# Kernel tuning notes

Hardware: AMD Instinct MI355X
Metric: run time of the kernel (lower is better)

Reference implementation:

```python
import jax, jax.numpy as jnp
import numpy as np

N_ORDERS = 4  # edge groups processed sequentially by EmulsionConv


def setup_inputs() -> dict:
    key = jax.random.key(0)
    ks = jax.random.split(key, 12)
    N, E, D_IN, H, D_OUT, ED = 50000, 800000, 10, 64, 10, 1
    s = 0.1
    return {
        "x": jax.random.normal(ks[0], (N, D_IN), jnp.float32),
        "edge_index": jax.random.randint(ks[1], (2, E), 0, N, jnp.int32),
        "edge_features": jax.random.normal(ks[2], (E, ED), jnp.float32),
        "lin0_w": jax.random.normal(ks[3], (D_IN, H), jnp.float32) * s,
        "lin0_b": jnp.zeros((H,), jnp.float32),
        "lin1_w": jax.random.normal(ks[4], (H, H), jnp.float32) * s,
        "lin1_b": jnp.zeros((H,), jnp.float32),
        "lin2_w": jax.random.normal(ks[5], (H, H), jnp.float32) * s,
        "lin2_b": jnp.zeros((H,), jnp.float32),
        "em_w": jax.random.normal(ks[6], (3, 2 * H + ED, H), jnp.float32) * s,
        "em_b": jnp.zeros((3, H), jnp.float32),
        "ec_w": jax.random.normal(ks[7], (3, 2 * H, H), jnp.float32) * s,
        "ec_b": jnp.zeros((3, H), jnp.float32),
        "out_w": jax.random.normal(ks[8], (H, D_OUT), jnp.float32) * s,
        "out_b": jnp.zeros((D_OUT,), jnp.float32),
    }


def _emulsion_conv(x, edge_index, edge_features, w, b):
    # Sequential per-order gather -> MLP message -> scatter-add; direction=0 (aggregate at source).
    N = x.shape[0]
    E = edge_index.shape[1]
    per = E // N_ORDERS
    for i in range(N_ORDERS):
        sl = slice(i * per, (i + 1) * per)
        src = edge_index[0, sl]
        dst = edge_index[1, sl]
        x_j = x[src]  # [per, H]
        x_i = x[dst]  # [per, H]
        msg = jnp.concatenate([x_i, x_j - x_i, edge_features[sl]], axis=1)
        msg = jax.nn.relu(msg @ w + b)
        agg = jax.ops.segment_sum(msg, src, num_segments=N)
        x = (x + agg) / 2.0
    return x


def _edge_conv(x, edge_index, w, b):
    # EdgeConv: nn([x_i, x_j - x_i]) with max aggregation at target nodes.
    N = x.shape[0]
    src, dst = edge_index[0], edge_index[1]
    x_i = x[dst]
    x_j = x[src]
    msg = jax.nn.relu(jnp.concatenate([x_i, x_j - x_i], axis=1) @ w + b)
    agg = jax.ops.segment_max(msg, dst, num_segments=N)
    return jnp.where(jnp.isfinite(agg), agg, 0.0)  # empty segments -> 0


def reference(x, edge_index, edge_features,
              lin0_w, lin0_b, lin1_w, lin1_b, lin2_w, lin2_b,
              em_w, em_b, ec_w, ec_b, out_w, out_b):
    lin_ws = [lin0_w, lin1_w, lin2_w]
    lin_bs = [lin0_b, lin1_b, lin2_b]
    for i in range(3):
        x = jax.nn.relu(x @ lin_ws[i] + lin_bs[i])
        x = _emulsion_conv(x, edge_index, edge_features, em_w[i], em_b[i])
    for i in range(3):
        x = _edge_conv(x, edge_index, ec_w[i], ec_b[i])
    return x @ out_w + out_b
```

## Files before the change

kernel.cpp:

```cpp
#include <hip/hip_runtime.h>
#include <hip/hip_fp16.h>


#define NN 50000
#define NE 800000
#define PER 200000
#define HD 64
#define NKEY 250112

typedef _Float16 half8 __attribute__((ext_vector_type(8)));
typedef float float4v __attribute__((ext_vector_type(4)));

__global__ __launch_bounds__(256) void count_kernel(
        const int* __restrict__ ei, int* __restrict__ cnt,
        uchar2* __restrict__ rank) {
    int e = blockIdx.x * 256 + threadIdx.x;
    if (e >= NE) return;
    int src = ei[e];
    int dst = ei[NE + e];
    int o = e / PER;
    int r1 = atomicAdd(&cnt[o * NN + src], 1);
    int r2 = atomicAdd(&cnt[4 * NN + dst], 1);
    rank[e] = make_uchar2((unsigned char)r1, (unsigned char)r2);
}

__global__ __launch_bounds__(256) void scan_blk(
        const int* __restrict__ cnt, int* __restrict__ bsum) {
    __shared__ int s[256];
    int t = threadIdx.x;
    int i = blockIdx.x * 256 + t;
    int c = (i < NKEY) ? cnt[i] : 0;
    s[t] = c; __syncthreads();
    for (int d = 1; d < 256; d <<= 1) {
        int v = (t >= d) ? s[t - d] : 0;
        __syncthreads(); s[t] += v; __syncthreads();
    }
    if (t == 255) bsum[blockIdx.x] = s[255];
}

__global__ __launch_bounds__(1024) void scan_top(
        const int* __restrict__ bsum, int* __restrict__ bofs, int nb) {
    __shared__ int s[1024];
    int t = threadIdx.x;
    int c = (t < nb) ? bsum[t] : 0;
    s[t] = c; __syncthreads();
    for (int d = 1; d < 1024; d <<= 1) {
        int v = (t >= d) ? s[t - d] : 0;
        __syncthreads(); s[t] += v; __syncthreads();
    }
    if (t < nb) bofs[t] = s[t] - c;
}

__global__ __launch_bounds__(256) void scan_fin(
        const int* __restrict__ cnt, const int* __restrict__ bofs,
        int* __restrict__ ofs) {
    __shared__ int s[256];
    int t = threadIdx.x;
    int i = blockIdx.x * 256 + t;
    int c = (i < NKEY) ? cnt[i] : 0;
    s[t] = c; __syncthreads();
    for (int d = 1; d < 256; d <<= 1) {
        int v = (t >= d) ? s[t - d] : 0;
        __syncthreads(); s[t] += v; __syncthreads();
    }
    if (i < NKEY) ofs[i] = bofs[blockIdx.x] + s[t] - c;
}

__global__ __launch_bounds__(256) void fill_kernel(
        const int* __restrict__ ei, const float* __restrict__ ef,
        const int* __restrict__ ofs, const uchar2* __restrict__ rank,
        unsigned* __restrict__ em_val, int* __restrict__ ec_val) {
    int e = blockIdx.x * 256 + threadIdx.x;
    if (e >= NE) return;
    int src = ei[e];
    int dst = ei[NE + e];
    int o = e / PER;
    uchar2 r = rank[e];
    int p1 = ofs[o * NN + src] + r.x;
    unsigned short eb = __half_as_ushort(__float2half_rn(ef[e]));
    em_val[p1] = ((unsigned)dst << 16) | (unsigned)eb;
    int p2 = ofs[4 * NN + dst] + r.y - NE;
    ec_val[p2] = src;
}

__global__ __launch_bounds__(256) void prep_w(
        const float* __restrict__ em_w, const float* __restrict__ ec_w,
        _Float16* __restrict__ wh) {
    int idx = blockIdx.x * 256 + threadIdx.x;
    int mat = idx >> 12, pos = idx & 4095;
    int n = pos >> 6, k = pos & 63;
    float val;
    if (mat < 3)      { const float* B = em_w + mat * 129 * 64;     val = B[k*64+n] - B[(64+k)*64+n]; }
    else if (mat < 6) { const float* B = em_w + (mat-3) * 129 * 64; val = B[(64+k)*64+n]; }
    else if (mat < 9) { const float* B = ec_w + (mat-6) * 128 * 64; val = B[k*64+n] - B[(64+k)*64+n]; }
    else              { const float* B = ec_w + (mat-9) * 128 * 64; val = B[(64+k)*64+n]; }
    _Float16 h = (_Float16)val;
    _Float16 l = (_Float16)(val - (float)h);
    wh[(size_t)mat * 4096 + n * 64 + k] = h;
    wh[(size_t)(12 + mat) * 4096 + n * 64 + k] = l;
}

template<int K>
__global__ __launch_bounds__(256) void lin_kernel(
        const float* __restrict__ xin,
        const float* __restrict__ W, const float* __restrict__ bias,
        float* __restrict__ xout) {
    __shared__ float xs[64][K + 1];
    int t = threadIdx.x;
    int n0 = blockIdx.x * 64;
    for (int idx = t; idx < 64 * K; idx += 256) {
        int n = idx / K, k = idx - n * K;
        int g = n0 + n;
        xs[n][k] = (g < NN) ? xin[(size_t)g * K + k] : 0.f;
    }
    __syncthreads();
    int ng = t >> 4;
    int f0 = (t & 15) * 4;
    float acc[4][4] = {};
    for (int k = 0; k < K; ++k) {
        float4 w4 = *(const float4*)&W[k * HD + f0];
        #pragma unroll
        for (int j = 0; j < 4; ++j) {
            float xv = xs[ng * 4 + j][k];
            acc[j][0] += xv * w4.x; acc[j][1] += xv * w4.y;
            acc[j][2] += xv * w4.z; acc[j][3] += xv * w4.w;
        }
    }
    float4 b4 = *(const float4*)&bias[f0];
    #pragma unroll
    for (int j = 0; j < 4; ++j) {
        int g = n0 + ng * 4 + j;
        if (g < NN) {
            float4 o;
            o.x = fmaxf(acc[j][0] + b4.x, 0.f);
            o.y = fmaxf(acc[j][1] + b4.y, 0.f);
            o.z = fmaxf(acc[j][2] + b4.z, 0.f);
            o.w = fmaxf(acc[j][3] + b4.w, 0.f);
            *(float4*)&xout[(size_t)g * HD + f0] = o;
        }
    }
}

__global__ __launch_bounds__(256) void uv_mfma(
        const float* __restrict__ x,
        const _Float16* __restrict__ Wuh, const _Float16* __restrict__ Wul,
        const _Float16* __restrict__ Wvh, const _Float16* __restrict__ Wvl,
        const float* __restrict__ bias,
        _Float16* __restrict__ u, _Float16* __restrict__ v) {
    __shared__ _Float16 xh[64 * 72], xl[64 * 72];
    __shared__ _Float16 wuh[64 * 72], wul[64 * 72];
    __shared__ _Float16 wvh[64 * 72], wvl[64 * 72];
    __shared__ _Float16 rp[4 * 16 * 72];
    int t = threadIdx.x;
    int n0 = blockIdx.x * 64;

    {
        int node = t >> 2, k0 = (t & 3) * 16;
        int g = n0 + node;
        float f[16];
        if (g < NN) {
            const float4* xr = (const float4*)&x[(size_t)g * HD + k0];
            *(float4*)&f[0] = xr[0]; *(float4*)&f[4] = xr[1];
            *(float4*)&f[8] = xr[2]; *(float4*)&f[12] = xr[3];
        } else {
            #pragma unroll
            for (int j = 0; j < 16; ++j) f[j] = 0.f;
        }
        half8 h0, h1, l0, l1;
        #pragma unroll
        for (int j = 0; j < 8; ++j) {
            _Float16 h = (_Float16)f[j];
            h0[j] = h; l0[j] = (_Float16)(f[j] - (float)h);
            _Float16 g2 = (_Float16)f[j + 8];
            h1[j] = g2; l1[j] = (_Float16)(f[j + 8] - (float)g2);
        }
        *(half8*)&xh[node * 72 + k0] = h0; *(half8*)&xh[node * 72 + k0 + 8] = h1;
        *(half8*)&xl[node * 72 + k0] = l0; *(half8*)&xl[node * 72 + k0 + 8] = l1;
    }
    {
        int n = t >> 2, c = (t & 3) * 16;
        *(half8*)&wuh[n * 72 + c]     = *(const half8*)&Wuh[n * 64 + c];
        *(half8*)&wuh[n * 72 + c + 8] = *(const half8*)&Wuh[n * 64 + c + 8];
        *(half8*)&wul[n * 72 + c]     = *(const half8*)&Wul[n * 64 + c];
        *(half8*)&wul[n * 72 + c + 8] = *(const half8*)&Wul[n * 64 + c + 8];
        *(half8*)&wvh[n * 72 + c]     = *(const half8*)&Wvh[n * 64 + c];
        *(half8*)&wvh[n * 72 + c + 8] = *(const half8*)&Wvh[n * 64 + c + 8];
        *(half8*)&wvl[n * 72 + c]     = *(const half8*)&Wvl[n * 64 + c];
        *(half8*)&wvl[n * 72 + c + 8] = *(const half8*)&Wvl[n * 64 + c + 8];
    }
    __syncthreads();

    int w = t >> 6, lane = t & 63;
    int quad = lane >> 4, l16 = lane & 15;
    int m0 = w * 16;
    half8 ah0 = *(half8*)&xh[(m0 + l16) * 72 + quad * 8];
    half8 ah1 = *(half8*)&xh[(m0 + l16) * 72 + 32 + quad * 8];
    half8 al0 = *(half8*)&xl[(m0 + l16) * 72 + quad * 8];
    half8 al1 = *(half8*)&xl[(m0 + l16) * 72 + 32 + quad * 8];

    float4v au[4], av[4];
    #pragma unroll
    for (int nt = 0; nt < 4; ++nt) {
        int n = nt * 16 + l16;
        half8 bh0 = *(half8*)&wuh[n * 72 + quad * 8];
        half8 bh1 = *(half8*)&wuh[n * 72 + 32 + quad * 8];
        half8 bl0 = *(half8*)&wul[n * 72 + quad * 8];
        half8 bl1 = *(half8*)&wul[n * 72 + 32 + quad * 8];
        float4v acc = {0.f, 0.f, 0.f, 0.f};
        acc = __builtin_amdgcn_mfma_f32_16x16x32_f16(ah0, bh0, acc, 0, 0, 0);
        acc = __builtin_amdgcn_mfma_f32_16x16x32_f16(ah1, bh1, acc, 0, 0, 0);
        acc = __builtin_amdgcn_mfma_f32_16x16x32_f16(al0, bh0, acc, 0, 0, 0);
        acc = __builtin_amdgcn_mfma_f32_16x16x32_f16(al1, bh1, acc, 0, 0, 0);
        acc = __builtin_amdgcn_mfma_f32_16x16x32_f16(ah0, bl0, acc, 0, 0, 0);
        acc = __builtin_amdgcn_mfma_f32_16x16x32_f16(ah1, bl1, acc, 0, 0, 0);
        au[nt] = acc;
        half8 ch0 = *(half8*)&wvh[n * 72 + quad * 8];
        half8 ch1 = *(half8*)&wvh[n * 72 + 32 + quad * 8];
        half8 cl0 = *(half8*)&wvl[n * 72 + quad * 8];
        half8 cl1 = *(half8*)&wvl[n * 72 + 32 + quad * 8];
        float4v accv = {0.f, 0.f, 0.f, 0.f};
        accv = __builtin_amdgcn_mfma_f32_16x16x32_f16(ah0, ch0, accv, 0, 0, 0);
        accv = __builtin_amdgcn_mfma_f32_16x16x32_f16(ah1, ch1, accv, 0, 0, 0);
        accv = __builtin_amdgcn_mfma_f32_16x16x32_f16(al0, ch0, accv, 0, 0, 0);
        accv = __builtin_amdgcn_mfma_f32_16x16x32_f16(al1, ch1, accv, 0, 0, 0);
        accv = __builtin_amdgcn_mfma_f32_16x16x32_f16(ah0, cl0, accv, 0, 0, 0);
        accv = __builtin_amdgcn_mfma_f32_16x16x32_f16(ah1, cl1, accv, 0, 0, 0);
        av[nt] = accv;
    }

    _Float16* rpw = &rp[w * 16 * 72];
    #pragma unroll
    for (int nt = 0; nt < 4; ++nt) {
        float bn = bias[nt * 16 + l16];
        #pragma unroll
        for (int r = 0; r < 4; ++r)
            rpw[(quad * 4 + r) * 72 + nt * 16 + l16] = (_Float16)(au[nt][r] + bn);
    }
    int mr = lane >> 2, cr = (lane & 3) * 16;
    int gr = n0 + m0 + mr;
    if (gr < NN) {
        *(half8*)&u[(size_t)gr * HD + cr]     = *(half8*)&rpw[mr * 72 + cr];
        *(half8*)&u[(size_t)gr * HD + cr + 8] = *(half8*)&rpw[mr * 72 + cr + 8];
    }
    #pragma unroll
    for (int nt = 0; nt < 4; ++nt) {
        #pragma unroll
        for (int r = 0; r < 4; ++r)
            rpw[(quad * 4 + r) * 72 + nt * 16 + l16] = (_Float16)(av[nt][r]);
    }
    if (gr < NN) {
        *(half8*)&v[(size_t)gr * HD + cr]     = *(half8*)&rpw[mr * 72 + cr];
        *(half8*)&v[(size_t)gr * HD + cr + 8] = *(half8*)&rpw[mr * 72 + cr + 8];
    }
}

__device__ __forceinline__ void load_h8(const __half* p, float* o) {
    float4 r = *(const float4*)p;
    __half2 h0 = *reinterpret_cast<__half2*>(&r.x);
    __half2 h1 = *reinterpret_cast<__half2*>(&r.y);
    __half2 h2 = *reinterpret_cast<__half2*>(&r.z);
    __half2 h3 = *reinterpret_cast<__half2*>(&r.w);
    float2 f0 = __half22float2(h0), f1 = __half22float2(h1);
    float2 f2 = __half22float2(h2), f3 = __half22float2(h3);
    o[0] = f0.x; o[1] = f0.y; o[2] = f1.x; o[3] = f1.y;
    o[4] = f2.x; o[5] = f2.y; o[6] = f3.x; o[7] = f3.y;
}

__global__ __launch_bounds__(256) void em_edge(
        const unsigned* __restrict__ em_val, const int* __restrict__ ofs,
        const __half* __restrict__ u, const __half* __restrict__ v,
        const float* __restrict__ we, float* __restrict__ x, int order) {
    int t = threadIdx.x;
    int node = blockIdx.x * 32 + (t >> 3);
    if (node >= NN) return;
    int f0 = (t & 7) * 8;
    int key = order * NN + node;
    int s0 = ofs[key], s1 = ofs[key + 1];
    float vn[8], wef[8], acc[8] = {};
    load_h8(&v[(size_t)node * HD + f0], vn);
    *(float4*)&wef[0] = *(const float4*)&we[f0];
    *(float4*)&wef[4] = *(const float4*)&we[f0 + 4];
    int p = s0;
    for (; p + 2 <= s1; p += 2) {
        unsigned e0 = em_val[p], e1 = em_val[p + 1];
        float u0[8], u1[8];
        load_h8(&u[(size_t)(e0 >> 16) * HD + f0], u0);
        load_h8(&u[(size_t)(e1 >> 16) * HD + f0], u1);
        float ef0 = __half2float(__ushort_as_half((unsigned short)(e0 & 0xffff)));
        float ef1 = __half2float(__ushort_as_half((unsigned short)(e1 & 0xffff)));
        #pragma unroll
        for (int j = 0; j < 8; ++j) {
            acc[j] += fmaxf(u0[j] + vn[j] + ef0 * wef[j], 0.f)
                    + fmaxf(u1[j] + vn[j] + ef1 * wef[j], 0.f);
        }
    }
    if (p < s1) {
        unsigned e0 = em_val[p];
        float u0[8];
        load_h8(&u[(size_t)(e0 >> 16) * HD + f0], u0);
        float ef0 = __half2float(__ushort_as_half((unsigned short)(e0 & 0xffff)));
        #pragma unroll
        for (int j = 0; j < 8; ++j)
            acc[j] += fmaxf(u0[j] + vn[j] + ef0 * wef[j], 0.f);
    }
    float xr[8];
    *(float4*)&xr[0] = *(const float4*)&x[(size_t)node * HD + f0];
    *(float4*)&xr[4] = *(const float4*)&x[(size_t)node * HD + f0 + 4];
    #pragma unroll
    for (int j = 0; j < 8; ++j) xr[j] = (xr[j] + acc[j]) * 0.5f;
    *(float4*)&x[(size_t)node * HD + f0] = *(float4*)&xr[0];
    *(float4*)&x[(size_t)node * HD + f0 + 4] = *(float4*)&xr[4];
}

__global__ __launch_bounds__(256) void ec_edge(
        const int* __restrict__ ec_val, const int* __restrict__ ofs,
        const __half* __restrict__ u, const __half* __restrict__ v,
        float* __restrict__ x) {
    int t = threadIdx.x;
    int node = blockIdx.x * 32 + (t >> 3);
    if (node >= NN) return;
    int f0 = (t & 7) * 8;
    int s0 = ofs[4 * NN + node] - NE, s1 = ofs[4 * NN + node + 1] - NE;
    float un[8], m[8] = {};
    load_h8(&u[(size_t)node * HD + f0], un);
    int p = s0;
    for (; p + 2 <= s1; p += 2) {
        int i0 = ec_val[p], i1 = ec_val[p + 1];
        float v0[8], v1[8];
        load_h8(&v[(size_t)i0 * HD + f0], v0);
        load_h8(&v[(size_t)i1 * HD + f0], v1);
        #pragma unroll
        for (int j = 0; j < 8; ++j)
            m[j] = fmaxf(m[j], fmaxf(un[j] + v0[j], un[j] + v1[j]));
    }
    if (p < s1) {
        int i0 = ec_val[p];
        float v0[8];
        load_h8(&v[(size_t)i0 * HD + f0], v0);
        #pragma unroll
        for (int j = 0; j < 8; ++j) m[j] = fmaxf(m[j], un[j] + v0[j]);
    }
    *(float4*)&x[(size_t)node * HD + f0] = *(float4*)&m[0];
    *(float4*)&x[(size_t)node * HD + f0 + 4] = *(float4*)&m[4];
}

__global__ __launch_bounds__(256) void out_kernel(
        const float* __restrict__ x, const float* __restrict__ W,
        const float* __restrict__ bias, float* __restrict__ out) {
    int n = blockIdx.x * 256 + threadIdx.x;
    if (n >= NN) return;
    float xr[HD];
    #pragma unroll
    for (int k = 0; k < HD; k += 4) {
        float4 t4 = *(const float4*)&x[(size_t)n * HD + k];
        xr[k] = t4.x; xr[k + 1] = t4.y; xr[k + 2] = t4.z; xr[k + 3] = t4.w;
    }
    #pragma unroll
    for (int f = 0; f < 10; ++f) {
        float acc = bias[f];
        #pragma unroll
        for (int k = 0; k < HD; ++k) acc += xr[k] * W[k * 10 + f];
        out[(size_t)n * 10 + f] = acc;
    }
}

extern "C" void kernel_launch(void* const* d_in, const int* in_sizes, int n_in,
                              void* d_out, int out_size, void* d_ws, size_t ws_size,
                              hipStream_t stream) {
    const float* x_in  = (const float*)d_in[0];
    const int*   ei    = (const int*)d_in[1];
    const float* ef    = (const float*)d_in[2];
    const float* lw[3] = {(const float*)d_in[3], (const float*)d_in[5], (const float*)d_in[7]};
    const float* lb[3] = {(const float*)d_in[4], (const float*)d_in[6], (const float*)d_in[8]};
    const float* em_w  = (const float*)d_in[9];
    const float* em_b  = (const float*)d_in[10];
    const float* ec_w  = (const float*)d_in[11];
    const float* ec_b  = (const float*)d_in[12];
    const float* ow    = (const float*)d_in[13];
    const float* ob    = (const float*)d_in[14];
    float* out = (float*)d_out;

    char* wsb = (char*)d_ws;
    size_t off = 0;
    auto alloc = [&](size_t bytes) {
        void* p = wsb + off;
        off = (off + bytes + 255) & ~(size_t)255;
        return p;
    };
    float*     x      = (float*)alloc((size_t)NN * HD * 4);
    _Float16*  u      = (_Float16*)alloc((size_t)NN * HD * 2);
    _Float16*  v      = (_Float16*)alloc((size_t)NN * HD * 2);
    int*       cnt    = (int*)alloc((size_t)NKEY * 4);
    int*       ofs    = (int*)alloc((size_t)NKEY * 4);
    int*       bsum   = (int*)alloc((size_t)1024 * 4);
    int*       bofs   = (int*)alloc((size_t)1024 * 4);
    uchar2*    rank   = (uchar2*)alloc((size_t)NE * 2);
    unsigned*  em_val = (unsigned*)alloc((size_t)NE * 4);
    int*       ec_val = (int*)alloc((size_t)NE * 4);
    _Float16*  wh     = (_Float16*)alloc((size_t)24 * 4096 * 2);
    (void)ws_size; (void)in_sizes; (void)n_in; (void)out_size;

    const int gb_nodes = (NN + 63) / 64;
    const int gb_edges = (NE + 255) / 256;
    const int gb_n8    = (NN + 31) / 32;
    const int gb_keys  = NKEY / 256;

    hipMemsetAsync(cnt, 0, (size_t)NKEY * 4, stream);
    count_kernel<<<gb_edges, 256, 0, stream>>>(ei, cnt, rank);
    prep_w<<<192, 256, 0, stream>>>(em_w, ec_w, wh);
    scan_blk<<<gb_keys, 256, 0, stream>>>(cnt, bsum);
    scan_top<<<1, 1024, 0, stream>>>(bsum, bofs, gb_keys);
    scan_fin<<<gb_keys, 256, 0, stream>>>(cnt, bofs, ofs);
    fill_kernel<<<gb_edges, 256, 0, stream>>>(ei, ef, ofs, rank, em_val, ec_val);

    lin_kernel<10><<<gb_nodes, 256, 0, stream>>>(x_in, lw[0], lb[0], x);

    for (int i = 0; i < 3; ++i) {
        const _Float16* Wuh = wh + (size_t)i * 4096;
        const _Float16* Wvh = wh + (size_t)(3 + i) * 4096;
        const _Float16* Wul = wh + (size_t)(12 + i) * 4096;
        const _Float16* Wvl = wh + (size_t)(15 + i) * 4096;
        const float* bi = em_b + (size_t)i * HD;
        const float* we = em_w + (size_t)i * 129 * HD + 128 * HD;
        for (int o = 0; o < 4; ++o) {
            uv_mfma<<<gb_nodes, 256, 0, stream>>>(x, Wuh, Wul, Wvh, Wvl, bi, u, v);
            em_edge<<<gb_n8, 256, 0, stream>>>(em_val, ofs, (const __half*)u,
                                               (const __half*)v, we, x, o);
        }
        if (i < 2)
            lin_kernel<64><<<gb_nodes, 256, 0, stream>>>(x, lw[i + 1], lb[i + 1], x);
    }

    for (int j = 0; j < 3; ++j) {
        const _Float16* Wuh = wh + (size_t)(6 + j) * 4096;
        const _Float16* Wvh = wh + (size_t)(9 + j) * 4096;
        const _Float16* Wul = wh + (size_t)(18 + j) * 4096;
        const _Float16* Wvl = wh + (size_t)(21 + j) * 4096;
        const float* bj = ec_b + (size_t)j * HD;
        uv_mfma<<<gb_nodes, 256, 0, stream>>>(x, Wuh, Wul, Wvh, Wvl, bj, u, v);
        ec_edge<<<gb_n8, 256, 0, stream>>>(ec_val, ofs, (const __half*)u,
                                           (const __half*)v, x);
    }

    out_kernel<<<(NN + 255) / 256, 256, 0, stream>>>(x, ow, ob, out);
}
```

Before: 582.5 us.

## Fuse preprocessing kernels, merge scan passes, slim uv LDS, restructure edge max

Merges count, weight prep and the first linear layer into one launch, and merges the CSR fill with the first uv projection. The three-pass scan becomes two: each block sums its preceding block totals itself. The uv kernel loads x straight into registers instead of staging it through LDS, which cuts shared memory per block. The edge-conv max now reduces over v first and adds u once per node with a single ReLU, removing the per-edge add. These trade fewer launches and less LDS traffic for larger, branchy fused kernels and redundant prefix-sum reads in the scan.

```diff
diff --git a/kernel.cpp b/kernel.cpp
--- a/kernel.cpp
+++ b/kernel.cpp
@@ -7,21 +7,84 @@
 #define PER 200000
 #define HD 64
 #define NKEY 250112
+#define GB_CNT 3125
+#define GB_PREP 192
+#define GB_LIN 782
+#define GB_KEYS 977
 
 typedef _Float16 half8 __attribute__((ext_vector_type(8)));
 typedef float float4v __attribute__((ext_vector_type(4)));
 
-__global__ __launch_bounds__(256) void count_kernel(
+struct UvLds {
+    _Float16 wuh[64 * 72], wul[64 * 72], wvh[64 * 72], wvl[64 * 72];
+    _Float16 rp[4 * 16 * 72];
+};
+
+__global__ __launch_bounds__(256) void k_front(
         const int* __restrict__ ei, int* __restrict__ cnt,
-        uchar2* __restrict__ rank) {
-    int e = blockIdx.x * 256 + threadIdx.x;
-    if (e >= NE) return;
-    int src = ei[e];
-    int dst = ei[NE + e];
-    int o = e / PER;
-    int r1 = atomicAdd(&cnt[o * NN + src], 1);
-    int r2 = atomicAdd(&cnt[4 * NN + dst], 1);
-    rank[e] = make_uchar2((unsigned char)r1, (unsigned char)r2);
+        uchar2* __restrict__ rank,
+        const float* __restrict__ em_w, const float* __restrict__ ec_w,
+        _Float16* __restrict__ wh,
+        const float* __restrict__ xin, const float* __restrict__ W0,
+        const float* __restrict__ b0, float* __restrict__ x) {
+    __shared__ float xs[64][11];
+    int t = threadIdx.x;
+    if (blockIdx.x < GB_CNT) {
+        int e = blockIdx.x * 256 + t;
+        int src = ei[e];
+        int dst = ei[NE + e];
+        int o = e / PER;
+        int r1 = atomicAdd(&cnt[o * NN + src], 1);
+        int r2 = atomicAdd(&cnt[4 * NN + dst], 1);
+        rank[e] = make_uchar2((unsigned char)r1, (unsigned char)r2);
+    } else if (blockIdx.x < GB_CNT + GB_PREP) {
+        int idx = (blockIdx.x - GB_CNT) * 256 + t;
+        int mat = idx >> 12, pos = idx & 4095;
+        int n = pos >> 6, k = pos & 63;
+        float val;
+        if (mat < 3)      { const float* B = em_w + mat * 129 * 64;     val = B[k*64+n] - B[(64+k)*64+n]; }
+        else if (mat < 6) { const float* B = em_w + (mat-3) * 129 * 64; val = B[(64+k)*64+n]; }
+        else if (mat < 9) { const float* B = ec_w + (mat-6) * 128 * 64; val = B[k*64+n] - B[(64+k)*64+n]; }
+        else              { const float* B = ec_w + (mat-9) * 128 * 64; val = B[(64+k)*64+n]; }
+        _Float16 h = (_Float16)val;
+        _Float16 l = (_Float16)(val - (float)h);
+        wh[(size_t)mat * 4096 + n * 64 + k] = h;
+        wh[(size_t)(12 + mat) * 4096 + n * 64 + k] = l;
+    } else {
+        const int K = 10;
+        int n0 = (blockIdx.x - GB_CNT - GB_PREP) * 64;
+        for (int idx = t; idx < 64 * K; idx += 256) {
+            int n = idx / K, k = idx - n * K;
+            int g = n0 + n;
+            xs[n][k] = (g < NN) ? xin[(size_t)g * K + k] : 0.f;
+        }
+        __syncthreads();
+        int ng = t >> 4;
+        int f0 = (t & 15) * 4;
+        float acc[4][4] = {};
+        for (int k = 0; k < K; ++k) {
+            float4 w4 = *(const float4*)&W0[k * HD + f0];
+            #pragma unroll
+            for (int j = 0; j < 4; ++j) {
+                float xv = xs[ng * 4 + j][k];
+                acc[j][0] += xv * w4.x; acc[j][1] += xv * w4.y;
+                acc[j][2] += xv * w4.z; acc[j][3] += xv * w4.w;
+            }
+        }
+        float4 b4 = *(const float4*)&b0[f0];
+        #pragma unroll
+        for (int j = 0; j < 4; ++j) {
+            int g = n0 + ng * 4 + j;
+            if (g < NN) {
+                float4 o;
+                o.x = fmaxf(acc[j][0] + b4.x, 0.f);
+                o.y = fmaxf(acc[j][1] + b4.y, 0.f);
+                o.z = fmaxf(acc[j][2] + b4.z, 0.f);
+                o.w = fmaxf(acc[j][3] + b4.w, 0.f);
+                *(float4*)&x[(size_t)g * HD + f0] = o;
+            }
+        }
+    }
 }
 
 __global__ __launch_bounds__(256) void scan_blk(
@@ -38,174 +101,83 @@
     if (t == 255) bsum[blockIdx.x] = s[255];
 }
 
-__global__ __launch_bounds__(1024) void scan_top(
-        const int* __restrict__ bsum, int* __restrict__ bofs, int nb) {
-    __shared__ int s[1024];
-    int t = threadIdx.x;
-    int c = (t < nb) ? bsum[t] : 0;
-    s[t] = c; __syncthreads();
-    for (int d = 1; d < 1024; d <<= 1) {
-        int v = (t >= d) ? s[t - d] : 0;
-        __syncthreads(); s[t] += v; __syncthreads();
-    }
-    if (t < nb) bofs[t] = s[t] - c;
-}
-
-__global__ __launch_bounds__(256) void scan_fin(
-        const int* __restrict__ cnt, const int* __restrict__ bofs,
+__global__ __launch_bounds__(256) void scan_fin2(
+        const int* __restrict__ cnt, const int* __restrict__ bsum,
         int* __restrict__ ofs) {
     __shared__ int s[256];
     int t = threadIdx.x;
     int i = blockIdx.x * 256 + t;
+    int pre = 0;
+    for (int j = t; j < blockIdx.x; j += 256) pre += bsum[j];
+    s[t] = pre; __syncthreads();
+    for (int d = 128; d > 0; d >>= 1) {
+        if (t < d) s[t] += s[t + d];
+        __syncthreads();
+    }
+    int base = s[0];
+    __syncthreads();
     int c = (i < NKEY) ? cnt[i] : 0;
     s[t] = c; __syncthreads();
     for (int d = 1; d < 256; d <<= 1) {
         int v = (t >= d) ? s[t - d] : 0;
         __syncthreads(); s[t] += v; __syncthreads();
     }
-    if (i < NKEY) ofs[i] = bofs[blockIdx.x] + s[t] - c;
-}
-
-__global__ __launch_bounds__(256) void fill_kernel(
-        const int* __restrict__ ei, const float* __restrict__ ef,
-        const int* __restrict__ ofs, const uchar2* __restrict__ rank,
-        unsigned* __restrict__ em_val, int* __restrict__ ec_val) {
-    int e = blockIdx.x * 256 + threadIdx.x;
-    if (e >= NE) return;
-    int src = ei[e];
-    int dst = ei[NE + e];
-    int o = e / PER;
-    uchar2 r = rank[e];
-    int p1 = ofs[o * NN + src] + r.x;
-    unsigned short eb = __half_as_ushort(__float2half_rn(ef[e]));
-    em_val[p1] = ((unsigned)dst << 16) | (unsigned)eb;
-    int p2 = ofs[4 * NN + dst] + r.y - NE;
-    ec_val[p2] = src;
-}
-
-__global__ __launch_bounds__(256) void prep_w(
-        const float* __restrict__ em_w, const float* __restrict__ ec_w,
-        _Float16* __restrict__ wh) {
-    int idx = blockIdx.x * 256 + threadIdx.x;
-    int mat = idx >> 12, pos = idx & 4095;
-    int n = pos >> 6, k = pos & 63;
-    float val;
-    if (mat < 3)      { const float* B = em_w + mat * 129 * 64;     val = B[k*64+n] - B[(64+k)*64+n]; }
-    else if (mat < 6) { const float* B = em_w + (mat-3) * 129 * 64; val = B[(64+k)*64+n]; }
-    else if (mat < 9) { const float* B = ec_w + (mat-6) * 128 * 64; val = B[k*64+n] - B[(64+k)*64+n]; }
-    else              { const float* B = ec_w + (mat-9) * 128 * 64; val = B[(64+k)*64+n]; }
-    _Float16 h = (_Float16)val;
-    _Float16 l = (_Float16)(val - (float)h);
-    wh[(size_t)mat * 4096 + n * 64 + k] = h;
-    wh[(size_t)(12 + mat) * 4096 + n * 64 + k] = l;
-}
-
-template<int K>
-__global__ __launch_bounds__(256) void lin_kernel(
-        const float* __restrict__ xin,
-        const float* __restrict__ W, const float* __restrict__ bias,
-        float* __restrict__ xout) {
-    __shared__ float xs[64][K + 1];
-    int t = threadIdx.x;
-    int n0 = blockIdx.x * 64;
-    for (int idx = t; idx < 64 * K; idx += 256) {
-        int n = idx / K, k = idx - n * K;
-        int g = n0 + n;
-        xs[n][k] = (g < NN) ? xin[(size_t)g * K + k] : 0.f;
-    }
-    __syncthreads();
-    int ng = t >> 4;
-    int f0 = (t & 15) * 4;
-    float acc[4][4] = {};
-    for (int k = 0; k < K; ++k) {
-        float4 w4 = *(const float4*)&W[k * HD + f0];
-        #pragma unroll
-        for (int j = 0; j < 4; ++j) {
-            float xv = xs[ng * 4 + j][k];
-            acc[j][0] += xv * w4.x; acc[j][1] += xv * w4.y;
-            acc[j][2] += xv * w4.z; acc[j][3] += xv * w4.w;
-        }
-    }
-    float4 b4 = *(const float4*)&bias[f0];
-    #pragma unroll
-    for (int j = 0; j < 4; ++j) {
-        int g = n0 + ng * 4 + j;
-        if (g < NN) {
-            float4 o;
-            o.x = fmaxf(acc[j][0] + b4.x, 0.f);
-            o.y = fmaxf(acc[j][1] + b4.y, 0.f);
-            o.z = fmaxf(acc[j][2] + b4.z, 0.f);
-            o.w = fmaxf(acc[j][3] + b4.w, 0.f);
-            *(float4*)&xout[(size_t)g * HD + f0] = o;
-        }
-    }
-}
-
-__global__ __launch_bounds__(256) void uv_mfma(
-        const float* __restrict__ x,
+    if (i < NKEY) ofs[i] = base + s[t] - c;
+}
+
+__device__ __forceinline__ void uv_body(
+        UvLds& L, int bid, const float* __restrict__ x,
         const _Float16* __restrict__ Wuh, const _Float16* __restrict__ Wul,
         const _Float16* __restrict__ Wvh, const _Float16* __restrict__ Wvl,
         const float* __restrict__ bias,
         _Float16* __restrict__ u, _Float16* __restrict__ v) {
-    __shared__ _Float16 xh[64 * 72], xl[64 * 72];
-    __shared__ _Float16 wuh[64 * 72], wul[64 * 72];
-    __shared__ _Float16 wvh[64 * 72], wvl[64 * 72];
-    __shared__ _Float16 rp[4 * 16 * 72];
-    int t = threadIdx.x;
-    int n0 = blockIdx.x * 64;
-
+    int t = threadIdx.x;
+    int n0 = bid * 64;
     {
-        int node = t >> 2, k0 = (t & 3) * 16;
-        int g = n0 + node;
+        int n = t >> 2, c = (t & 3) * 16;
+        *(half8*)&L.wuh[n * 72 + c]     = *(const half8*)&Wuh[n * 64 + c];
+        *(half8*)&L.wuh[n * 72 + c + 8] = *(const half8*)&Wuh[n * 64 + c + 8];
+        *(half8*)&L.wul[n * 72 + c]     = *(const half8*)&Wul[n * 64 + c];
+        *(half8*)&L.wul[n * 72 + c + 8] = *(const half8*)&Wul[n * 64 + c + 8];
+        *(half8*)&L.wvh[n * 72 + c]     = *(const half8*)&Wvh[n * 64 + c];
+        *(half8*)&L.wvh[n * 72 + c + 8] = *(const half8*)&Wvh[n * 64 + c + 8];
+        *(half8*)&L.wvl[n * 72 + c]     = *(const half8*)&Wvl[n * 64 + c];
+        *(half8*)&L.wvl[n * 72 + c + 8] = *(const half8*)&Wvl[n * 64 + c + 8];
+    }
+    int w = t >> 6, lane = t & 63;
+    int quad = lane >> 4, l16 = lane & 15;
+    int m0 = w * 16;
+    int row = n0 + m0 + l16;
+    half8 ah0, ah1, al0, al1;
+    {
         float f[16];
-        if (g < NN) {
-            const float4* xr = (const float4*)&x[(size_t)g * HD + k0];
-            *(float4*)&f[0] = xr[0]; *(float4*)&f[4] = xr[1];
-            *(float4*)&f[8] = xr[2]; *(float4*)&f[12] = xr[3];
+        if (row < NN) {
+            const float4* p = (const float4*)&x[(size_t)row * HD + quad * 8];
+            *(float4*)&f[0] = p[0]; *(float4*)&f[4] = p[1];
+            const float4* q = (const float4*)&x[(size_t)row * HD + 32 + quad * 8];
+            *(float4*)&f[8] = q[0]; *(float4*)&f[12] = q[1];
         } else {
             #pragma unroll
             for (int j = 0; j < 16; ++j) f[j] = 0.f;
         }
-        half8 h0, h1, l0, l1;
         #pragma unroll
         for (int j = 0; j < 8; ++j) {
             _Float16 h = (_Float16)f[j];
-            h0[j] = h; l0[j] = (_Float16)(f[j] - (float)h);
-            _Float16 g2 = (_Float16)f[j + 8];
-            h1[j] = g2; l1[j] = (_Float16)(f[j + 8] - (float)g2);
-        }
-        *(half8*)&xh[node * 72 + k0] = h0; *(half8*)&xh[node * 72 + k0 + 8] = h1;
-        *(half8*)&xl[node * 72 + k0] = l0; *(half8*)&xl[node * 72 + k0 + 8] = l1;
-    }
-    {
-        int n = t >> 2, c = (t & 3) * 16;
-        *(half8*)&wuh[n * 72 + c]     = *(const half8*)&Wuh[n * 64 + c];
-        *(half8*)&wuh[n * 72 + c + 8] = *(const half8*)&Wuh[n * 64 + c + 8];
-        *(half8*)&wul[n * 72 + c]     = *(const half8*)&Wul[n * 64 + c];
-        *(half8*)&wul[n * 72 + c + 8] = *(const half8*)&Wul[n * 64 + c + 8];
-        *(half8*)&wvh[n * 72 + c]     = *(const half8*)&Wvh[n * 64 + c];
-        *(half8*)&wvh[n * 72 + c + 8] = *(const half8*)&Wvh[n * 64 + c + 8];
-        *(half8*)&wvl[n * 72 + c]     = *(const half8*)&Wvl[n * 64 + c];
-        *(half8*)&wvl[n * 72 + c + 8] = *(const half8*)&Wvl[n * 64 + c + 8];
+            ah0[j] = h; al0[j] = (_Float16)(f[j] - (float)h);
+            _Float16 h2 = (_Float16)f[j + 8];
+            ah1[j] = h2; al1[j] = (_Float16)(f[j + 8] - (float)h2);
+        }
     }
     __syncthreads();
-
-    int w = t >> 6, lane = t & 63;
-    int quad = lane >> 4, l16 = lane & 15;
-    int m0 = w * 16;
-    half8 ah0 = *(half8*)&xh[(m0 + l16) * 72 + quad * 8];
-    half8 ah1 = *(half8*)&xh[(m0 + l16) * 72 + 32 + quad * 8];
-    half8 al0 = *(half8*)&xl[(m0 + l16) * 72 + quad * 8];
-    half8 al1 = *(half8*)&xl[(m0 + l16) * 72 + 32 + quad * 8];
 
     float4v au[4], av[4];
     #pragma unroll
     for (int nt = 0; nt < 4; ++nt) {
         int n = nt * 16 + l16;
-        half8 bh0 = *(half8*)&wuh[n * 72 + quad * 8];
-        half8 bh1 = *(half8*)&wuh[n * 72 + 32 + quad * 8];
-        half8 bl0 = *(half8*)&wul[n * 72 + quad * 8];
-        half8 bl1 = *(half8*)&wul[n * 72 + 32 + quad * 8];
+        half8 bh0 = *(half8*)&L.wuh[n * 72 + quad * 8];
+        half8 bh1 = *(half8*)&L.wuh[n * 72 + 32 + quad * 8];
+        half8 bl0 = *(half8*)&L.wul[n * 72 + quad * 8];
+        half8 bl1 = *(half8*)&L.wul[n * 72 + 32 + quad * 8];
         float4v acc = {0.f, 0.f, 0.f, 0.f};
         acc = __builtin_amdgcn_mfma_f32_16x16x32_f16(ah0, bh0, acc, 0, 0, 0);
         acc = __builtin_amdgcn_mfma_f32_16x16x32_f16(ah1, bh1, acc, 0, 0, 0);
@@ -214,10 +186,10 @@
         acc = __builtin_amdgcn_mfma_f32_16x16x32_f16(ah0, bl0, acc, 0, 0, 0);
         acc = __builtin_amdgcn_mfma_f32_16x16x32_f16(ah1, bl1, acc, 0, 0, 0);
         au[nt] = acc;
-        half8 ch0 = *(half8*)&wvh[n * 72 + quad * 8];
-        half8 ch1 = *(half8*)&wvh[n * 72 + 32 + quad * 8];
-        half8 cl0 = *(half8*)&wvl[n * 72 + quad * 8];
-        half8 cl1 = *(half8*)&wvl[n * 72 + 32 + quad * 8];
+        half8 ch0 = *(half8*)&L.wvh[n * 72 + quad * 8];
+        half8 ch1 = *(half8*)&L.wvh[n * 72 + 32 + quad * 8];
+        half8 cl0 = *(half8*)&L.wvl[n * 72 + quad * 8];
+        half8 cl1 = *(half8*)&L.wvl[n * 72 + 32 + quad * 8];
         float4v accv = {0.f, 0.f, 0.f, 0.f};
         accv = __builtin_amdgcn_mfma_f32_16x16x32_f16(ah0, ch0, accv, 0, 0, 0);
         accv = __builtin_amdgcn_mfma_f32_16x16x32_f16(ah1, ch1, accv, 0, 0, 0);
@@ -228,7 +200,7 @@
         av[nt] = accv;
     }
 
-    _Float16* rpw = &rp[w * 16 * 72];
+    _Float16* rpw = &L.rp[w * 16 * 72];
     #pragma unroll
     for (int nt = 0; nt < 4; ++nt) {
         float bn = bias[nt * 16 + l16];
@@ -251,6 +223,42 @@
     if (gr < NN) {
         *(half8*)&v[(size_t)gr * HD + cr]     = *(half8*)&rpw[mr * 72 + cr];
         *(half8*)&v[(size_t)gr * HD + cr + 8] = *(half8*)&rpw[mr * 72 + cr + 8];
+    }
+}
+
+__global__ __launch_bounds__(256) void uv_slim(
+        const float* __restrict__ x,
+        const _Float16* __restrict__ Wuh, const _Float16* __restrict__ Wul,
+        const _Float16* __restrict__ Wvh, const _Float16* __restrict__ Wvl,
+        const float* __restrict__ bias,
+        _Float16* __restrict__ u, _Float16* __restrict__ v) {
+    __shared__ UvLds L;
+    uv_body(L, blockIdx.x, x, Wuh, Wul, Wvh, Wvl, bias, u, v);
+}
+
+__global__ __launch_bounds__(256) void k_fill_uv(
+        const int* __restrict__ ei, const float* __restrict__ ef,
+        const int* __restrict__ ofs, const uchar2* __restrict__ rank,
+        unsigned* __restrict__ em_val, int* __restrict__ ec_val,
+        const float* __restrict__ x,
+        const _Float16* __restrict__ Wuh, const _Float16* __restrict__ Wul,
+        const _Float16* __restrict__ Wvh, const _Float16* __restrict__ Wvl,
+        const float* __restrict__ bias,
+        _Float16* __restrict__ u, _Float16* __restrict__ v) {
+    __shared__ UvLds L;
+    if (blockIdx.x < GB_CNT) {
+        int e = blockIdx.x * 256 + threadIdx.x;
+        int src = ei[e];
+        int dst = ei[NE + e];
+        int o = e / PER;
+        uchar2 r = rank[e];
+        int p1 = ofs[o * NN + src] + r.x;
+        unsigned short eb = __half_as_ushort(__float2half_rn(ef[e]));
+        em_val[p1] = ((unsigned)dst << 16) | (unsigned)eb;
+        int p2 = ofs[4 * NN + dst] + r.y - NE;
+        ec_val[p2] = src;
+    } else {
+        uv_body(L, blockIdx.x - GB_CNT, x, Wuh, Wul, Wvh, Wvl, bias, u, v);
     }
 }
 
@@ -321,27 +329,79 @@
     if (node >= NN) return;
     int f0 = (t & 7) * 8;
     int s0 = ofs[4 * NN + node] - NE, s1 = ofs[4 * NN + node + 1] - NE;
-    float un[8], m[8] = {};
-    load_h8(&u[(size_t)node * HD + f0], un);
-    int p = s0;
-    for (; p + 2 <= s1; p += 2) {
-        int i0 = ec_val[p], i1 = ec_val[p + 1];
-        float v0[8], v1[8];
-        load_h8(&v[(size_t)i0 * HD + f0], v0);
-        load_h8(&v[(size_t)i1 * HD + f0], v1);
-        #pragma unroll
-        for (int j = 0; j < 8; ++j)
-            m[j] = fmaxf(m[j], fmaxf(un[j] + v0[j], un[j] + v1[j]));
-    }
-    if (p < s1) {
-        int i0 = ec_val[p];
-        float v0[8];
-        load_h8(&v[(size_t)i0 * HD + f0], v0);
-        #pragma unroll
-        for (int j = 0; j < 8; ++j) m[j] = fmaxf(m[j], un[j] + v0[j]);
-    }
-    *(float4*)&x[(size_t)node * HD + f0] = *(float4*)&m[0];
-    *(float4*)&x[(size_t)node * HD + f0 + 4] = *(float4*)&m[4];
+    float o[8];
+    if (s1 > s0) {
+        float m[8];
+        #pragma unroll
+        for (int j = 0; j < 8; ++j) m[j] = -3.0e38f;
+        int p = s0;
+        for (; p + 2 <= s1; p += 2) {
+            int i0 = ec_val[p], i1 = ec_val[p + 1];
+            float v0[8], v1[8];
+            load_h8(&v[(size_t)i0 * HD + f0], v0);
+            load_h8(&v[(size_t)i1 * HD + f0], v1);
+            #pragma unroll
+            for (int j = 0; j < 8; ++j)
+                m[j] = fmaxf(m[j], fmaxf(v0[j], v1[j]));
+        }
+        if (p < s1) {
+            int i0 = ec_val[p];
+            float v0[8];
+            load_h8(&v[(size_t)i0 * HD + f0], v0);
+            #pragma unroll
+            for (int j = 0; j < 8; ++j) m[j] = fmaxf(m[j], v0[j]);
+        }
+        float un[8];
+        load_h8(&u[(size_t)node * HD + f0], un);
+        #pragma unroll
+        for (int j = 0; j < 8; ++j) o[j] = fmaxf(un[j] + m[j], 0.f);
+    } else {
+        #pragma unroll
+        for (int j = 0; j < 8; ++j) o[j] = 0.f;
+    }
+    *(float4*)&x[(size_t)node * HD + f0] = *(float4*)&o[0];
+    *(float4*)&x[(size_t)node * HD + f0 + 4] = *(float4*)&o[4];
+}
+
+template<int K>
+__global__ __launch_bounds__(256) void lin_kernel(
+        const float* __restrict__ xin,
+        const float* __restrict__ W, const float* __restrict__ bias,
+        float* __restrict__ xout) {
+    __shared__ float xs[64][K + 1];
+    int t = threadIdx.x;
+    int n0 = blockIdx.x * 64;
+    for (int idx = t; idx < 64 * K; idx += 256) {
+        int n = idx / K, k = idx - n * K;
+        int g = n0 + n;
+        xs[n][k] = (g < NN) ? xin[(size_t)g * K + k] : 0.f;
+    }
+    __syncthreads();
+    int ng = t >> 4;
+    int f0 = (t & 15) * 4;
+    float acc[4][4] = {};
+    for (int k = 0; k < K; ++k) {
+        float4 w4 = *(const float4*)&W[k * HD + f0];
+        #pragma unroll
+        for (int j = 0; j < 4; ++j) {
+            float xv = xs[ng * 4 + j][k];
+            acc[j][0] += xv * w4.x; acc[j][1] += xv * w4.y;
+            acc[j][2] += xv * w4.z; acc[j][3] += xv * w4.w;
+        }
+    }
+    float4 b4 = *(const float4*)&bias[f0];
+    #pragma unroll
+    for (int j = 0; j < 4; ++j) {
+        int g = n0 + ng * 4 + j;
+        if (g < NN) {
+            float4 o;
+            o.x = fmaxf(acc[j][0] + b4.x, 0.f);
+            o.y = fmaxf(acc[j][1] + b4.y, 0.f);
+            o.z = fmaxf(acc[j][2] + b4.z, 0.f);
+            o.w = fmaxf(acc[j][3] + b4.w, 0.f);
+            *(float4*)&xout[(size_t)g * HD + f0] = o;
+        }
+    }
 }
 
 __global__ __launch_bounds__(256) void out_kernel(
@@ -393,27 +453,24 @@
     int*       cnt    = (int*)alloc((size_t)NKEY * 4);
     int*       ofs    = (int*)alloc((size_t)NKEY * 4);
     int*       bsum   = (int*)alloc((size_t)1024 * 4);
-    int*       bofs   = (int*)alloc((size_t)1024 * 4);
     uchar2*    rank   = (uchar2*)alloc((size_t)NE * 2);
     unsigned*  em_val = (unsigned*)alloc((size_t)NE * 4);
     int*       ec_val = (int*)alloc((size_t)NE * 4);
     _Float16*  wh     = (_Float16*)alloc((size_t)24 * 4096 * 2);
     (void)ws_size; (void)in_sizes; (void)n_in; (void)out_size;
 
-    const int gb_nodes = (NN + 63) / 64;
-    const int gb_edges = (NE + 255) / 256;
-    const int gb_n8    = (NN + 31) / 32;
-    const int gb_keys  = NKEY / 256;
+    const int gb_n8 = (NN + 31) / 32;
 
     hipMemsetAsync(cnt, 0, (size_t)NKEY * 4, stream);
-    count_kernel<<<gb_edges, 256, 0, stream>>>(ei, cnt, rank);
-    prep_w<<<192, 256, 0, stream>>>(em_w, ec_w, wh);
-    scan_blk<<<gb_keys, 256, 0, stream>>>(cnt, bsum);
-    scan_top<<<1, 1024, 0, stream>>>(bsum, bofs, gb_keys);
-    scan_fin<<<gb_keys, 256, 0, stream>>>(cnt, bofs, ofs);
-    fill_kernel<<<gb_edges, 256, 0, stream>>>(ei, ef, ofs, rank, em_val, ec_val);
-
-    lin_kernel<10><<<gb_nodes, 256, 0, stream>>>(x_in, lw[0], lb[0], x);
+    k_front<<<GB_CNT + GB_PREP + GB_LIN, 256, 0, stream>>>(
+        ei, cnt, rank, em_w, ec_w, wh, x_in, lw[0], lb[0], x);
+    scan_blk<<<GB_KEYS, 256, 0, stream>>>(cnt, bsum);
+    scan_fin2<<<GB_KEYS, 256, 0, stream>>>(cnt, bsum, ofs);
+
+    k_fill_uv<<<GB_CNT + GB_LIN, 256, 0, stream>>>(
+        ei, ef, ofs, rank, em_val, ec_val, x,
+        wh, wh + (size_t)12 * 4096, wh + (size_t)3 * 4096, wh + (size_t)15 * 4096,
+        em_b, u, v);
 
     for (int i = 0; i < 3; ++i) {
         const _Float16* Wuh = wh + (size_t)i * 4096;
@@ -423,12 +480,13 @@
         const float* bi = em_b + (size_t)i * HD;
         const float* we = em_w + (size_t)i * 129 * HD + 128 * HD;
         for (int o = 0; o < 4; ++o) {
-            uv_mfma<<<gb_nodes, 256, 0, stream>>>(x, Wuh, Wul, Wvh, Wvl, bi, u, v);
+            if (!(i == 0 && o == 0))
+                uv_slim<<<GB_LIN, 256, 0, stream>>>(x, Wuh, Wul, Wvh, Wvl, bi, u, v);
             em_edge<<<gb_n8, 256, 0, stream>>>(em_val, ofs, (const __half*)u,
                                                (const __half*)v, we, x, o);
         }
         if (i < 2)
-            lin_kernel<64><<<gb_nodes, 256, 0, stream>>>(x, lw[i + 1], lb[i + 1], x);
+            lin_kernel<64><<<GB_LIN, 256, 0, stream>>>(x, lw[i + 1], lb[i + 1], x);
     }
 
     for (int j = 0; j < 3; ++j) {
@@ -437,7 +495,7 @@
         const _Float16* Wul = wh + (size_t)(18 + j) * 4096;
         const _Float16* Wvl = wh + (size_t)(21 + j) * 4096;
         const float* bj = ec_b + (size_t)j * HD;
-        uv_mfma<<<gb_nodes, 256, 0, stream>>>(x, Wuh, Wul, Wvh, Wvl, bj, u, v);
+        uv_slim<<<GB_LIN, 256, 0, stream>>>(x, Wuh, Wul, Wvh, Wvl, bj, u, v);
         ec_edge<<<gb_n8, 256, 0, stream>>>(ec_val, ofs, (const __half*)u,
                                            (const __half*)v, x);
     }
```

Result: no change. 583.9 us (+0.2%).
